# Optimization experiments

Measured on AMD Instinct MI355X. Metric: run time of the kernel, lower is better.

The kernel has to match this reference:

```python
import jax, jax.numpy as jnp
import numpy as np

B, T, IN, OUT = 8, 2048, 2048, 2048

def setup_inputs() -> dict:
    key = jax.random.key(0)
    k1, k2, k3, k4 = jax.random.split(key, 4)
    x = jax.random.normal(k1, (B, T, IN), dtype=jnp.float32)
    # ternary weights in {-1, 0, 1}, stored as int8 like the torch buffer
    w_q = (jax.random.randint(k2, (OUT, IN), 0, 3) - 1).astype(jnp.int8)
    # per-output-channel power-of-two exponents (downscaling), int8 buffer
    s_exp = jax.random.randint(k3, (OUT,), -8, 1).astype(jnp.int8)
    bias = jax.random.normal(k4, (OUT,), dtype=jnp.float32) * 0.1
    return {"x": x, "w_q": w_q, "s_exp": s_exp, "bias": bias}

def reference(x, w_q, s_exp, bias):
    # F.linear(x, w_q.float()): y[b,t,o] = sum_i x[b,t,i] * w_q[o,i]
    y = jnp.einsum('bti,oi->bto', x, w_q.astype(x.dtype))
    # torch.ldexp(y, s_exp): y * 2**s_exp, broadcast over last dim
    y = y * jnp.exp2(s_exp.astype(jnp.float32)).astype(x.dtype)
    return y + bias
```

## Files before the change

kernel.cpp:

```cpp
#include <hip/hip_runtime.h>

#define MT 16384
#define NT 2048
#define KT 2048
#define BM 128
#define BN 128
#define BK 64

typedef __attribute__((ext_vector_type(8))) short short8;
typedef __attribute__((ext_vector_type(4))) float f32x4;
typedef __attribute__((ext_vector_type(8))) unsigned short ushort8;
typedef __attribute__((ext_vector_type(4))) unsigned short ushort4v;

__device__ __forceinline__ unsigned short f32_bf16(float f) {
    union { float f; unsigned u; } v; v.f = f;
    return (unsigned short)((v.u + 0x7FFFu + ((v.u >> 16) & 1u)) >> 16);
}


__global__ __launch_bounds__(256) void cvt_kernel(const float* __restrict__ x,
                                                  const int* __restrict__ w,
                                                  unsigned short* __restrict__ xb,
                                                  unsigned short* __restrict__ wb) {
    const int b = blockIdx.x;
    if (b < MT * KT / 2048) {
        size_t i = ((size_t)b * 256 + threadIdx.x) * 8;
        float4 v0 = *(const float4*)(x + i);
        float4 v1 = *(const float4*)(x + i + 4);
        ushort8 o;
        o[0] = f32_bf16(v0.x); o[1] = f32_bf16(v0.y); o[2] = f32_bf16(v0.z); o[3] = f32_bf16(v0.w);
        o[4] = f32_bf16(v1.x); o[5] = f32_bf16(v1.y); o[6] = f32_bf16(v1.z); o[7] = f32_bf16(v1.w);
        *(ushort8*)(xb + i) = o;
    } else {
        size_t i = ((size_t)(b - MT * KT / 2048) * 256 + threadIdx.x) * 8;
        int4 v0 = *(const int4*)(w + i);
        int4 v1 = *(const int4*)(w + i + 4);
        ushort8 o;
        o[0] = f32_bf16((float)v0.x); o[1] = f32_bf16((float)v0.y);
        o[2] = f32_bf16((float)v0.z); o[3] = f32_bf16((float)v0.w);
        o[4] = f32_bf16((float)v1.x); o[5] = f32_bf16((float)v1.y);
        o[6] = f32_bf16((float)v1.z); o[7] = f32_bf16((float)v1.w);
        *(ushort8*)(wb + i) = o;
    }
}


__device__ __forceinline__ int swz(int row, int c) {
    return row * 8 + ((c + row) & 7);
}

template <bool PRE>
__global__ __launch_bounds__(256) void gemm_bt(
    const unsigned short* __restrict__ Abf, const unsigned short* __restrict__ Bbf,
    const float* __restrict__ Af32, const int* __restrict__ Wi32,
    const int* __restrict__ sexp, const float* __restrict__ bias,
    float* __restrict__ C)
{
    __shared__ unsigned short As[BM * BK];
    __shared__ unsigned short Bs[BN * BK];

    const int tid  = threadIdx.x;
    const int row0 = blockIdx.y * BM;
    const int col0 = blockIdx.x * BN;
    const int lane = tid & 63;
    const int wave = tid >> 6;
    const int wm = wave >> 1, wn = wave & 1;
    const int q = lane >> 4, r = lane & 15;

    f32x4 acc[4][4] = {};

    for (int k0 = 0; k0 < KT; k0 += BK) {
        if constexpr (PRE) {
            #pragma unroll
            for (int ii = 0; ii < 4; ++ii) {
                const int s   = tid + ii * 256;
                const int row = s >> 3;
                const int cg  = ((s & 7) - row) & 7;
                const unsigned short* ga =
                    Abf + (size_t)(row0 + row) * KT + k0 + cg * 8;
                __builtin_amdgcn_global_load_lds(
                    (const __attribute__((address_space(1))) unsigned int*)ga,
                    (__attribute__((address_space(3))) unsigned int*)(As + (size_t)(ii * 256 + wave * 64) * 8),
                    16, 0, 0);
                const unsigned short* gb =
                    Bbf + (size_t)(col0 + row) * KT + k0 + cg * 8;
                __builtin_amdgcn_global_load_lds(
                    (const __attribute__((address_space(1))) unsigned int*)gb,
                    (__attribute__((address_space(3))) unsigned int*)(Bs + (size_t)(ii * 256 + wave * 64) * 8),
                    16, 0, 0);
            }
        } else {
            #pragma unroll
            for (int ii = 0; ii < 8; ++ii) {
                const int s  = tid + ii * 256;
                const int rw = s >> 4, c4 = s & 15;
                const int ch = c4 >> 1, hf = c4 & 1;
                const int ps = ((ch + rw) & 7) * 8 + hf * 4;
                float4 v = *(const float4*)(Af32 + (size_t)(row0 + rw) * KT + k0 + c4 * 4);
                ushort4v oa;
                oa[0] = f32_bf16(v.x); oa[1] = f32_bf16(v.y);
                oa[2] = f32_bf16(v.z); oa[3] = f32_bf16(v.w);
                *(ushort4v*)(As + rw * BK + ps) = oa;
                int4 w4 = *(const int4*)(Wi32 + (size_t)(col0 + rw) * KT + k0 + c4 * 4);
                ushort4v ob;
                ob[0] = f32_bf16((float)w4.x); ob[1] = f32_bf16((float)w4.y);
                ob[2] = f32_bf16((float)w4.z); ob[3] = f32_bf16((float)w4.w);
                *(ushort4v*)(Bs + rw * BK + ps) = ob;
            }
        }
        __syncthreads();

        #pragma unroll
        for (int h = 0; h < 2; ++h) {
            short8 a[4], b[4];
            #pragma unroll
            for (int i = 0; i < 4; ++i)
                a[i] = *(const short8*)(As + swz(wm * 64 + i * 16 + r, h * 4 + q) * 8);
            #pragma unroll
            for (int j = 0; j < 4; ++j)
                b[j] = *(const short8*)(Bs + swz(wn * 64 + j * 16 + r, h * 4 + q) * 8);
            #pragma unroll
            for (int i = 0; i < 4; ++i)
                #pragma unroll
                for (int j = 0; j < 4; ++j)
                    acc[i][j] = __builtin_amdgcn_mfma_f32_16x16x32_bf16(a[i], b[j], acc[i][j], 0, 0, 0);
        }
        __syncthreads();
    }

    #pragma unroll
    for (int j = 0; j < 4; ++j) {
        const int n  = col0 + wn * 64 + j * 16 + r;
        const float sc = ldexpf(1.0f, sexp[n]);
        const float bs = bias[n];
        #pragma unroll
        for (int i = 0; i < 4; ++i) {
            const int m = row0 + wm * 64 + i * 16 + q * 4;
            float* cp = C + (size_t)m * NT + n;
            #pragma unroll
            for (int t = 0; t < 4; ++t)
                cp[(size_t)t * NT] = acc[i][j][t] * sc + bs;
        }
    }
}

extern "C" void kernel_launch(void* const* d_in, const int* in_sizes, int n_in,
                              void* d_out, int out_size, void* d_ws, size_t ws_size,
                              hipStream_t stream) {
    const float* x    = (const float*)d_in[0];
    const int*   wq   = (const int*)d_in[1];
    const int*   se   = (const int*)d_in[2];
    const float* bias = (const float*)d_in[3];
    float* out = (float*)d_out;

    const size_t xb_elems = (size_t)MT * KT;
    const size_t wb_elems = (size_t)NT * KT;
    dim3 grid(NT / BN, MT / BM);

    if (ws_size >= (xb_elems + wb_elems) * sizeof(unsigned short)) {
        unsigned short* xb = (unsigned short*)d_ws;
        unsigned short* wb = xb + xb_elems;
        cvt_kernel<<<(int)((xb_elems + wb_elems) / (256 * 8)), 256, 0, stream>>>(x, wq, xb, wb);
        gemm_bt<true><<<grid, 256, 0, stream>>>(xb, wb, nullptr, nullptr, se, bias, out);
    } else {
        gemm_bt<false><<<grid, 256, 0, stream>>>(nullptr, nullptr, x, wq, se, bias, out);
    }
}
```

Baseline: 391.2 us.

## Replace bf16 GEMM with 256x256 tiled, double-buffered 8-phase pipelined kernel

The precomputed-bf16 GEMM path moves from 128x128 tiles with 256 threads to 256x256 tiles with 512 threads (8 waves). It double-buffers LDS via global_load_lds and splits each k-tile into four phases that interleave async staging, barriers and MFMA bursts at raised priority. The aim is to hide global-load latency and raise arithmetic intensity per LDS byte. In exchange it needs 128 KB of LDS and many more accumulator registers, which may limit occupancy, and the hand-tuned vmcnt waits are fragile. The fallback fp32 path is kept as a separate kernel.

```diff
diff --git a/kernel.cpp b/kernel.cpp
--- a/kernel.cpp
+++ b/kernel.cpp
@@ -3,9 +3,11 @@
 #define MT 16384
 #define NT 2048
 #define KT 2048
-#define BM 128
-#define BN 128
+#define BM 256
+#define BN 256
 #define BK 64
+#define NKT (KT / BK)
+#define THREADS 512
 
 typedef __attribute__((ext_vector_type(8))) short short8;
 typedef __attribute__((ext_vector_type(4))) float f32x4;
@@ -45,23 +47,165 @@
 }
 
 
-__device__ __forceinline__ int swz(int row, int c) {
-    return row * 8 + ((c + row) & 7);
-}
-
-template <bool PRE>
-__global__ __launch_bounds__(256) void gemm_bt(
+__global__ __launch_bounds__(THREADS, 2) void gemm_8ph(
     const unsigned short* __restrict__ Abf, const unsigned short* __restrict__ Bbf,
+    const int* __restrict__ sexp, const float* __restrict__ bias,
+    float* __restrict__ C)
+{
+    __shared__ unsigned short As[2 * 2048 * 8];
+    __shared__ unsigned short Bs[2 * 2048 * 8];
+
+    const int tid  = threadIdx.x;
+    const int bn   = blockIdx.x;
+    const int bm   = blockIdx.y;
+    const int brow0 = bm * BM;
+    const int bcol0 = bn * BN;
+    const int lane = tid & 63;
+    const int wave = tid >> 6;
+    const int wm = wave >> 2;
+    const int wn = wave & 3;
+    const int q = lane >> 4, r = lane & 15;
+
+    size_t aoff[2][2], boff[2][2];
+    #pragma unroll
+    for (int h = 0; h < 2; ++h)
+        #pragma unroll
+        for (int ii = 0; ii < 2; ++ii) {
+            const int s   = h * 1024 + ii * 512 + tid;
+            const int row = s >> 3;
+            const int cg  = ((s & 7) - row) & 7;
+            aoff[h][ii] = (size_t)(brow0 + row) * KT + cg * 8;
+            boff[h][ii] = (size_t)(bcol0 + row) * KT + cg * 8;
+        }
+
+#define GLDS(srcp, dstp)                                                            \
+    __builtin_amdgcn_global_load_lds(                                               \
+        (const __attribute__((address_space(1))) unsigned int*)(srcp),              \
+        (__attribute__((address_space(3))) unsigned int*)(dstp), 16, 0, 0)
+
+    auto stageA = [&](int tile, int h) {
+        const int buf = tile & 1;
+        const size_t k = (size_t)tile * BK;
+        GLDS(Abf + aoff[h][0] + k, As + buf * 16384 + (h * 1024 + wave * 64) * 8);
+        GLDS(Abf + aoff[h][1] + k, As + buf * 16384 + (h * 1024 + 512 + wave * 64) * 8);
+    };
+    auto stageB = [&](int tile, int h) {
+        const int buf = tile & 1;
+        const size_t k = (size_t)tile * BK;
+        GLDS(Bbf + boff[h][0] + k, Bs + buf * 16384 + (h * 1024 + wave * 64) * 8);
+        GLDS(Bbf + boff[h][1] + k, Bs + buf * 16384 + (h * 1024 + 512 + wave * 64) * 8);
+    };
+
+    f32x4 acc[8][4] = {};
+    short8 a[2][2];
+    short8 b[4][2];
+
+    auto ldA = [&](int buf, int p) {
+        const unsigned short* base = As + buf * 16384;
+        #pragma unroll
+        for (int u = 0; u < 2; ++u) {
+            const int row = (4 * p + 2 * u + wm) * 16 + r;
+            #pragma unroll
+            for (int kh = 0; kh < 2; ++kh)
+                a[u][kh] = *(const short8*)(base + row * 64 + ((kh * 4 + q + row) & 7) * 8);
+        }
+    };
+    auto ldB = [&](int buf) {
+        const unsigned short* base = Bs + buf * 16384;
+        #pragma unroll
+        for (int j = 0; j < 4; ++j) {
+            const int row = (4 * wn + j) * 16 + r;
+            #pragma unroll
+            for (int kh = 0; kh < 2; ++kh)
+                b[j][kh] = *(const short8*)(base + row * 64 + ((kh * 4 + q + row) & 7) * 8);
+        }
+    };
+    auto mma = [&](int p) {
+        #pragma unroll
+        for (int kh = 0; kh < 2; ++kh)
+            #pragma unroll
+            for (int u = 0; u < 2; ++u)
+                #pragma unroll
+                for (int j = 0; j < 4; ++j)
+                    acc[2 * p + u][j] = __builtin_amdgcn_mfma_f32_16x16x32_bf16(
+                        a[u][kh], b[j][kh], acc[2 * p + u][j], 0, 0, 0);
+    };
+
+#define PHASE(buf, p, STAGE_STMT, WAIT_STMT) do {          \
+        ldA(buf, p);                                       \
+        if ((p) == 0) ldB(buf);                            \
+        STAGE_STMT;                                        \
+        __builtin_amdgcn_s_barrier();                      \
+        asm volatile("s_waitcnt lgkmcnt(0)");              \
+        __builtin_amdgcn_sched_barrier(0);                 \
+        __builtin_amdgcn_s_setprio(1);                     \
+        mma(p);                                            \
+        __builtin_amdgcn_s_setprio(0);                     \
+        WAIT_STMT;                                         \
+        __builtin_amdgcn_s_barrier();                      \
+    } while (0)
+
+    stageB(0, 0); stageB(0, 1); stageA(0, 0); stageA(0, 1);
+    asm volatile("s_waitcnt vmcnt(4)" ::: "memory");
+    stageB(1, 0); stageA(1, 0); stageB(1, 1);
+    asm volatile("s_waitcnt vmcnt(6)" ::: "memory");
+    __builtin_amdgcn_s_barrier();
+
+    #pragma unroll 1
+    for (int i = 0; i < NKT / 2 - 1; ++i) {
+        const int t1 = 2 * i + 1, t2 = 2 * i + 2, t3 = 2 * i + 3;
+        PHASE(0, 0, stageA(t1, 1), (void)0);
+        PHASE(0, 1, stageB(t2, 0), (void)0);
+        PHASE(0, 2, stageA(t2, 0), (void)0);
+        PHASE(0, 3, stageB(t2, 1), asm volatile("s_waitcnt vmcnt(6)" ::: "memory"));
+        PHASE(1, 0, stageA(t2, 1), (void)0);
+        PHASE(1, 1, stageB(t3, 0), (void)0);
+        PHASE(1, 2, stageA(t3, 0), (void)0);
+        PHASE(1, 3, stageB(t3, 1), asm volatile("s_waitcnt vmcnt(6)" ::: "memory"));
+    }
+
+    PHASE(0, 0, stageA(NKT - 1, 1), (void)0);
+    PHASE(0, 1, (void)0, asm volatile("s_waitcnt vmcnt(4)" ::: "memory"));
+    PHASE(0, 2, (void)0, asm volatile("s_waitcnt vmcnt(2)" ::: "memory"));
+    PHASE(0, 3, (void)0, asm volatile("s_waitcnt vmcnt(0)" ::: "memory"));
+    PHASE(1, 0, (void)0, (void)0);
+    PHASE(1, 1, (void)0, (void)0);
+    PHASE(1, 2, (void)0, (void)0);
+    PHASE(1, 3, (void)0, (void)0);
+
+#undef PHASE
+#undef GLDS
+
+    #pragma unroll
+    for (int j = 0; j < 4; ++j) {
+        const int n  = bcol0 + (4 * wn + j) * 16 + r;
+        const float sc = ldexpf(1.0f, sexp[n]);
+        const float bs = bias[n];
+        #pragma unroll
+        for (int f = 0; f < 8; ++f) {
+            const int m = brow0 + (2 * f + wm) * 16 + q * 4;
+            float* cp = C + (size_t)m * NT + n;
+            #pragma unroll
+            for (int t = 0; t < 4; ++t)
+                cp[(size_t)t * NT] = acc[f][j][t] * sc + bs;
+        }
+    }
+}
+
+
+__device__ __forceinline__ int swzf(int row, int c) { return row * 8 + ((c + row) & 7); }
+
+__global__ __launch_bounds__(256) void gemm_fb(
     const float* __restrict__ Af32, const int* __restrict__ Wi32,
     const int* __restrict__ sexp, const float* __restrict__ bias,
     float* __restrict__ C)
 {
-    __shared__ unsigned short As[BM * BK];
-    __shared__ unsigned short Bs[BN * BK];
+    __shared__ unsigned short As[128 * 64];
+    __shared__ unsigned short Bs[128 * 64];
 
     const int tid  = threadIdx.x;
-    const int row0 = blockIdx.y * BM;
-    const int col0 = blockIdx.x * BN;
+    const int row0 = blockIdx.y * 128;
+    const int col0 = blockIdx.x * 128;
     const int lane = tid & 63;
     const int wave = tid >> 6;
     const int wm = wave >> 1, wn = wave & 1;
@@ -69,56 +213,34 @@
 
     f32x4 acc[4][4] = {};
 
-    for (int k0 = 0; k0 < KT; k0 += BK) {
-        if constexpr (PRE) {
-            #pragma unroll
-            for (int ii = 0; ii < 4; ++ii) {
-                const int s   = tid + ii * 256;
-                const int row = s >> 3;
-                const int cg  = ((s & 7) - row) & 7;
-                const unsigned short* ga =
-                    Abf + (size_t)(row0 + row) * KT + k0 + cg * 8;
-                __builtin_amdgcn_global_load_lds(
-                    (const __attribute__((address_space(1))) unsigned int*)ga,
-                    (__attribute__((address_space(3))) unsigned int*)(As + (size_t)(ii * 256 + wave * 64) * 8),
-                    16, 0, 0);
-                const unsigned short* gb =
-                    Bbf + (size_t)(col0 + row) * KT + k0 + cg * 8;
-                __builtin_amdgcn_global_load_lds(
-                    (const __attribute__((address_space(1))) unsigned int*)gb,
-                    (__attribute__((address_space(3))) unsigned int*)(Bs + (size_t)(ii * 256 + wave * 64) * 8),
-                    16, 0, 0);
-            }
-        } else {
-            #pragma unroll
-            for (int ii = 0; ii < 8; ++ii) {
-                const int s  = tid + ii * 256;
-                const int rw = s >> 4, c4 = s & 15;
-                const int ch = c4 >> 1, hf = c4 & 1;
-                const int ps = ((ch + rw) & 7) * 8 + hf * 4;
-                float4 v = *(const float4*)(Af32 + (size_t)(row0 + rw) * KT + k0 + c4 * 4);
-                ushort4v oa;
-                oa[0] = f32_bf16(v.x); oa[1] = f32_bf16(v.y);
-                oa[2] = f32_bf16(v.z); oa[3] = f32_bf16(v.w);
-                *(ushort4v*)(As + rw * BK + ps) = oa;
-                int4 w4 = *(const int4*)(Wi32 + (size_t)(col0 + rw) * KT + k0 + c4 * 4);
-                ushort4v ob;
-                ob[0] = f32_bf16((float)w4.x); ob[1] = f32_bf16((float)w4.y);
-                ob[2] = f32_bf16((float)w4.z); ob[3] = f32_bf16((float)w4.w);
-                *(ushort4v*)(Bs + rw * BK + ps) = ob;
-            }
+    for (int k0 = 0; k0 < KT; k0 += 64) {
+        #pragma unroll
+        for (int ii = 0; ii < 8; ++ii) {
+            const int s  = tid + ii * 256;
+            const int rw = s >> 4, c4 = s & 15;
+            const int ch = c4 >> 1, hf = c4 & 1;
+            const int ps = ((ch + rw) & 7) * 8 + hf * 4;
+            float4 v = *(const float4*)(Af32 + (size_t)(row0 + rw) * KT + k0 + c4 * 4);
+            ushort4v oa;
+            oa[0] = f32_bf16(v.x); oa[1] = f32_bf16(v.y);
+            oa[2] = f32_bf16(v.z); oa[3] = f32_bf16(v.w);
+            *(ushort4v*)(As + rw * 64 + ps) = oa;
+            int4 w4 = *(const int4*)(Wi32 + (size_t)(col0 + rw) * KT + k0 + c4 * 4);
+            ushort4v ob;
+            ob[0] = f32_bf16((float)w4.x); ob[1] = f32_bf16((float)w4.y);
+            ob[2] = f32_bf16((float)w4.z); ob[3] = f32_bf16((float)w4.w);
+            *(ushort4v*)(Bs + rw * 64 + ps) = ob;
         }
         __syncthreads();
-
         #pragma unroll
         for (int h = 0; h < 2; ++h) {
             short8 a[4], b[4];
             #pragma unroll
             for (int i = 0; i < 4; ++i)
-                a[i] = *(const short8*)(As + swz(wm * 64 + i * 16 + r, h * 4 + q) * 8);
+                a[i] = *(const short8*)(As + swzf(wm * 64 + i * 16 + r, h * 4 + q) * 8);
             #pragma unroll
             for (int j = 0; j < 4; ++j)
-                b[j] = *(const short8*)(Bs + swz(wn * 64 + j * 16 + r, h * 4 + q) * 8);
+                b[j] = *(const short8*)(Bs + swzf(wn * 64 + j * 16 + r, h * 4 + q) * 8);
             #pragma unroll
             for (int i = 0; i < 4; ++i)
                 #pragma unroll
@@ -155,14 +277,15 @@
 
     const size_t xb_elems = (size_t)MT * KT;
     const size_t wb_elems = (size_t)NT * KT;
-    dim3 grid(NT / BN, MT / BM);
 
     if (ws_size >= (xb_elems + wb_elems) * sizeof(unsigned short)) {
         unsigned short* xb = (unsigned short*)d_ws;
         unsigned short* wb = xb + xb_elems;
         cvt_kernel<<<(int)((xb_elems + wb_elems) / (256 * 8)), 256, 0, stream>>>(x, wq, xb, wb);
-        gemm_bt<true><<<grid, 256, 0, stream>>>(xb, wb, nullptr, nullptr, se, bias, out);
+        dim3 grid(NT / BN, MT / BM);
+        gemm_8ph<<<grid, THREADS, 0, stream>>>(xb, wb, se, bias, out);
     } else {
-        gemm_bt<false><<<grid, 256, 0, stream>>>(nullptr, nullptr, x, wq, se, bias, out);
-    }
-}
+        dim3 fgrid(NT / 128, MT / 128);
+        gemm_fb<<<fgrid, 256, 0, stream>>>(x, wq, se, bias, out);
+    }
+}
```

After: 364.5 us. 1.07x faster.
